# Kernel tuning notes

Measured on AMD Instinct MI355X. Metric: run time of the kernel, lower is better.

Reference implementation:

```python
import jax, jax.numpy as jnp
import numpy as np


def setup_inputs() -> dict:
    key = jax.random.key(0)
    ks = jax.random.split(key, 8)
    B, C, H, W = 4, 512, 64, 64
    O = 64  # output_size for f/g projections
    x = jax.random.normal(ks[0], (B, C, H, W), dtype=jnp.float32)
    s = 0.02
    f_w = jax.random.normal(ks[1], (O, C), dtype=jnp.float32) * s
    f_b = jnp.zeros((O,), dtype=jnp.float32)
    g_w = jax.random.normal(ks[2], (O, C), dtype=jnp.float32) * s
    g_b = jnp.zeros((O,), dtype=jnp.float32)
    h_w = jax.random.normal(ks[3], (C, C), dtype=jnp.float32) * s
    h_b = jnp.zeros((C,), dtype=jnp.float32)
    gamma = jnp.float32(0.5)  # torch init is 0.0; nonzero to exercise the attention path
    return {"x": x, "f_w": f_w, "f_b": f_b, "g_w": g_w, "g_b": g_b,
            "h_w": h_w, "h_b": h_b, "gamma": gamma}


def reference(x, f_w, f_b, g_w, g_b, h_w, h_b, gamma):
    B, C, Hh, Ww = x.shape
    N = Hh * Ww
    # 1x1 convs == per-pixel linear projections
    xf = x.reshape(B, C, N)                                   # [B,C,N]
    f = jnp.einsum('oc,bcn->bon', f_w, xf) + f_b[None, :, None]  # [B,O,N]
    g = jnp.einsum('oc,bcn->bon', g_w, xf) + g_b[None, :, None]  # [B,O,N]
    h = jnp.einsum('oc,bcn->bon', h_w, xf) + h_b[None, :, None]  # [B,C,N]
    # scores[b,i,j] = <f[:, i], g[:, j]>  (f transposed to [B,N,O] then bmm with g)
    scores = jnp.einsum('boi,boj->bij', f, g)                 # [B,N,N]
    # NOTE: original uses nn.Softmax(dim=1) -> normalize over the i (first N) axis
    sm = jax.nn.softmax(scores, axis=1)                       # [B,N,N]
    attn = jnp.einsum('bcn,bnm->bcm', h, sm)                  # [B,C,N]
    out = gamma * attn.reshape(B, C, Hh, Ww) + x
    return out
```

## Files before the change

### kernel.cpp

```cpp
#include <hip/hip_runtime.h>


#define N_PIX 4096
#define C_IN  512

typedef __attribute__((ext_vector_type(8)))  short bf16x8;
typedef __attribute__((ext_vector_type(16))) float f32x16;
typedef __attribute__((ext_vector_type(8)))  int   i32x8;

__device__ __forceinline__ float fexp2(float x) {
    return __builtin_amdgcn_exp2f(x);
}

__device__ inline unsigned int f2bf(float f) {
    union { float f; unsigned u; } x; x.f = f;
    unsigned r = x.u + 0x7FFFu + ((x.u >> 16) & 1u);
    return r >> 16;
}

__device__ __forceinline__ unsigned cvt_pk_bf16(float a, float b) {
#if __has_builtin(__builtin_amdgcn_cvt_pk_bf16_f32)
    auto r = __builtin_amdgcn_cvt_pk_bf16_f32(a, b);
    unsigned u; __builtin_memcpy(&u, &r, 4); return u;
#else
    return f2bf(a) | (f2bf(b) << 16);
#endif
}

__device__ __forceinline__ unsigned pk_fp8x4(float a, float b, float c, float d) {
    int v = 0;
    v = __builtin_amdgcn_cvt_pk_fp8_f32(a, b, v, false);
    v = __builtin_amdgcn_cvt_pk_fp8_f32(c, d, v, true);
    return (unsigned)v;
}

__global__ __launch_bounds__(256) void pack_w(
    const float* __restrict__ f_w, const float* __restrict__ g_w,
    const float* __restrict__ h_w, unsigned short* __restrict__ wall)
{
    __shared__ __align__(16) unsigned short Ls[32 * 520];
    const int t  = threadIdx.x;
    const int tt = blockIdx.x;
    const float* W; int rbase;
    if (tt < 2)      { W = f_w; rbase = tt * 32; }
    else if (tt < 4) { W = g_w; rbase = (tt - 2) * 32; }
    else             { W = h_w; rbase = (tt - 4) * 32; }
    const float fs = (tt < 2) ? 1.442695041f : 1.0f;

    #pragma unroll
    for (int k = 0; k < 16; ++k) {
        const int off = (t + k * 256) * 4;
        const int row = off >> 9, col = off & 511;
        float4 v = *(const float4*)&W[(size_t)(rbase + row) * C_IN + col];
        uint2 pk; pk.x = cvt_pk_bf16(v.x * fs, v.y * fs); pk.y = cvt_pk_bf16(v.z * fs, v.w * fs);
        *(uint2*)&Ls[row * 520 + col] = pk;
    }
    __syncthreads();
    #pragma unroll
    for (int j = 0; j < 8; ++j) {
        const int o = t + j * 256;
        const int q = o >> 6, lq = o & 63;
        const int row = lq & 31, c0 = q * 16 + (lq >> 5) * 8;
        uint4 pk = *(const uint4*)&Ls[row * 520 + c0];
        *(uint4*)&wall[(size_t)tt * 16384 + (size_t)o * 8] = pk;
    }
}

__global__ __launch_bounds__(512, 4) void proj_kernel(
    const float* __restrict__ x,
    const unsigned short* __restrict__ wall,
    const float* __restrict__ f_b, const float* __restrict__ g_b,
    const float* __restrict__ h_b,
    unsigned short* __restrict__ fa, unsigned short* __restrict__ gbuf,
    unsigned char* __restrict__ ha)
{
    __shared__ __align__(16) unsigned short Xf[2][8192];
    const int t    = threadIdx.x;
    const int w    = t >> 6;
    const int l    = t & 63;
    const int half = l >> 5;
    const int tx = t & 15;
    const int ty = t >> 4;
    const int c0 = ty * 2;
    const int qs = c0 >> 4;
    const int woff = (c0 & 7);
    const int hfs = (c0 >> 3) & 1;

    const int blk = blockIdx.x;

    if (blk < 256) {
        const int b  = blk >> 6;
        const int nb = blk & 63;
        const int n0g = nb * 64;
        const int n0 = tx * 4;

        f32x16 acc[2][2];
        #pragma unroll
        for (int j = 0; j < 2; ++j)
            #pragma unroll
            for (int s = 0; s < 2; ++s)
                #pragma unroll
                for (int r = 0; r < 16; ++r) acc[j][s][r] = 0.f;

        const unsigned short* wp0 = wall + (size_t)(4 + w * 2) * 16384 + (size_t)l * 8;
        const unsigned short* wp1 = wp0 + 16384;
        bf16x8 wc0 = *(const bf16x8*)wp0;
        bf16x8 wc1 = *(const bf16x8*)wp1;

        float4 v0 = *(const float4*)&x[((size_t)(b * C_IN + c0)) * N_PIX + n0g + n0];
        float4 v1 = *(const float4*)&x[((size_t)(b * C_IN + c0 + 1)) * N_PIX + n0g + n0];

        for (int it = 0; it < 8; ++it) {
            {
                unsigned short* xb = &Xf[it & 1][0];
                const float a0[4] = {v0.x, v0.y, v0.z, v0.w};
                const float a1[4] = {v1.x, v1.y, v1.z, v1.w};
                #pragma unroll
                for (int j = 0; j < 4; ++j) {
                    const int n = n0 + j;
                    const int off = ((n >> 5) * 4 + qs) * 512
                                  + ((n & 31) + 32 * hfs) * 8 + woff;
                    *(unsigned*)&xb[off] = cvt_pk_bf16(a0[j], a1[j]);
                }
            }
            if (it < 7) {
                v0 = *(const float4*)&x[((size_t)(b * C_IN + (it + 1) * 64 + c0)) * N_PIX + n0g + n0];
                v1 = *(const float4*)&x[((size_t)(b * C_IN + (it + 1) * 64 + c0 + 1)) * N_PIX + n0g + n0];
            }
            __syncthreads();
            const unsigned short* xb = &Xf[it & 1][0];
            #pragma unroll
            for (int q = 0; q < 4; ++q) {
                const int qn = (it * 4 + q + 1) & 31;
                bf16x8 wn0 = *(const bf16x8*)(wp0 + (size_t)qn * 512);
                bf16x8 wn1 = *(const bf16x8*)(wp1 + (size_t)qn * 512);
                bf16x8 x0 = *(const bf16x8*)&xb[(0 * 4 + q) * 512 + l * 8];
                bf16x8 x1 = *(const bf16x8*)&xb[(1 * 4 + q) * 512 + l * 8];
                acc[0][0] = __builtin_amdgcn_mfma_f32_32x32x16_bf16(x0, wc0, acc[0][0], 0, 0, 0);
                acc[0][1] = __builtin_amdgcn_mfma_f32_32x32x16_bf16(x1, wc0, acc[0][1], 0, 0, 0);
                acc[1][0] = __builtin_amdgcn_mfma_f32_32x32x16_bf16(x0, wc1, acc[1][0], 0, 0, 0);
                acc[1][1] = __builtin_amdgcn_mfma_f32_32x32x16_bf16(x1, wc1, acc[1][1], 0, 0, 0);
                wc0 = wn0; wc1 = wn1;
            }
            __syncthreads();
        }

        const int nt_ = nb >> 1, kt_ = nb & 1;
        #pragma unroll
        for (int j = 0; j < 2; ++j) {
            const int ctile = w * 2 + j;
            const int ch = ctile * 32 + (l & 31);
            const float hb = h_b[ch];
            unsigned char* hdst = ha
                + (((size_t)(b * 16 + ctile) * 32 + nt_) * 2 + kt_) * 2048
                + (size_t)(l & 31) * 32 + 16 * half;
            #pragma unroll
            for (int ns = 0; ns < 2; ++ns) {
                uint4 pk4;
                pk4.x = pk_fp8x4(acc[j][ns][0]  + hb, acc[j][ns][1]  + hb,
                                 acc[j][ns][2]  + hb, acc[j][ns][3]  + hb);
                pk4.y = pk_fp8x4(acc[j][ns][4]  + hb, acc[j][ns][5]  + hb,
                                 acc[j][ns][6]  + hb, acc[j][ns][7]  + hb);
                pk4.z = pk_fp8x4(acc[j][ns][8]  + hb, acc[j][ns][9]  + hb,
                                 acc[j][ns][10] + hb, acc[j][ns][11] + hb);
                pk4.w = pk_fp8x4(acc[j][ns][12] + hb, acc[j][ns][13] + hb,
                                 acc[j][ns][14] + hb, acc[j][ns][15] + hb);
                *(uint4*)&hdst[ns * 1024] = pk4;
            }
        }
    } else {
        const int blk2 = blk - 256;
        const int b   = blk2 >> 5;
        const int nb2 = blk2 & 31;
        const int n0g = nb2 * 128;
        const int tt    = w & 3;
        const int npair = w >> 2;

        f32x16 acc[2];
        #pragma unroll
        for (int s = 0; s < 2; ++s)
            #pragma unroll
            for (int r = 0; r < 16; ++r) acc[s][r] = 0.f;

        const unsigned short* wpf = wall + (size_t)tt * 16384 + (size_t)l * 8;
        bf16x8 wcf = *(const bf16x8*)wpf;

        float4 v00 = *(const float4*)&x[((size_t)(b * C_IN + c0)) * N_PIX + n0g + tx * 4];
        float4 v10 = *(const float4*)&x[((size_t)(b * C_IN + c0 + 1)) * N_PIX + n0g + tx * 4];
        float4 v01 = *(const float4*)&x[((size_t)(b * C_IN + c0)) * N_PIX + n0g + 64 + tx * 4];
        float4 v11 = *(const float4*)&x[((size_t)(b * C_IN + c0 + 1)) * N_PIX + n0g + 64 + tx * 4];

        for (int it = 0; it < 8; ++it) {
            {
                unsigned short* xb = &Xf[it & 1][0];
                const float a00[4] = {v00.x, v00.y, v00.z, v00.w};
                const float a10[4] = {v10.x, v10.y, v10.z, v10.w};
                const float a01[4] = {v01.x, v01.y, v01.z, v01.w};
                const float a11[4] = {v11.x, v11.y, v11.z, v11.w};
                #pragma unroll
                for (int j = 0; j < 4; ++j) {
                    const int n = tx * 4 + j;
                    const int off0 = ((n >> 5) * 4 + qs) * 512
                                   + ((n & 31) + 32 * hfs) * 8 + woff;
                    *(unsigned*)&xb[off0] = cvt_pk_bf16(a00[j], a10[j]);
                    const int n2 = 64 + n;
                    const int off1 = ((n2 >> 5) * 4 + qs) * 512
                                   + ((n2 & 31) + 32 * hfs) * 8 + woff;
                    *(unsigned*)&xb[off1] = cvt_pk_bf16(a01[j], a11[j]);
                }
            }
            if (it < 7) {
                const size_t rb = (size_t)(b * C_IN + (it + 1) * 64 + c0) * N_PIX + n0g;
                v00 = *(const float4*)&x[rb + tx * 4];
                v10 = *(const float4*)&x[rb + N_PIX + tx * 4];
                v01 = *(const float4*)&x[rb + 64 + tx * 4];
                v11 = *(const float4*)&x[rb + N_PIX + 64 + tx * 4];
            }
            __syncthreads();
            const unsigned short* xb = &Xf[it & 1][0];
            #pragma unroll
            for (int q = 0; q < 4; ++q) {
                const int qn = (it * 4 + q + 1) & 31;
                bf16x8 wnf = *(const bf16x8*)(wpf + (size_t)qn * 512);
                bf16x8 x0 = *(const bf16x8*)&xb[((npair * 2 + 0) * 4 + q) * 512 + l * 8];
                bf16x8 x1 = *(const bf16x8*)&xb[((npair * 2 + 1) * 4 + q) * 512 + l * 8];
                acc[0] = __builtin_amdgcn_mfma_f32_32x32x16_bf16(wcf, x0, acc[0], 0, 0, 0);
                acc[1] = __builtin_amdgcn_mfma_f32_32x32x16_bf16(wcf, x1, acc[1], 0, 0, 0);
                wcf = wnf;
            }
            __syncthreads();
        }

        unsigned short* buf = (tt < 2) ? fa : gbuf;
        const float* bias = (tt < 2) ? f_b : g_b;
        const float bscale = (tt < 2) ? 1.442695041f : 1.0f;
        #pragma unroll
        for (int s = 0; s < 2; ++s) {
            const int ntile = nb2 * 4 + npair * 2 + s;
            #pragma unroll
            for (int j2 = 0; j2 < 4; ++j2) {
                const int o_base = (tt & 1) * 32 + 8 * j2 + 4 * half;
                float4 bv = *(const float4*)&bias[o_base];
                bv.x *= bscale; bv.y *= bscale; bv.z *= bscale; bv.w *= bscale;
                const int q  = o_base >> 4;
                const int lp = (l & 31) + 32 * (j2 & 1);
                uint2 pk;
                pk.x = cvt_pk_bf16(acc[s][4 * j2 + 0] + bv.x, acc[s][4 * j2 + 1] + bv.y);
                pk.y = cvt_pk_bf16(acc[s][4 * j2 + 2] + bv.z, acc[s][4 * j2 + 3] + bv.w);
                size_t off = (((size_t)(b * 128 + ntile) * 4 + q) * 64 + lp) * 8 + 4 * half;
                *(uint2*)&buf[off] = pk;
            }
        }
    }
}

__global__ __launch_bounds__(512, 4) void attn_kernel(
    const unsigned short* __restrict__ fa,
    const unsigned short* __restrict__ gbuf,
    const unsigned char* __restrict__ ha,
    const float* __restrict__ x,
    const float* __restrict__ gamma_p,
    float* __restrict__ out)
{
    __shared__ __align__(16) unsigned char Ebuf[2][64 * 136];
    __shared__ float den_part[4][64];
    __shared__ float den_inv[64];

    const int t    = threadIdx.x;
    const int w    = t >> 6;
    const int l    = t & 63;
    const int lane = l & 31;
    const int half = l >> 5;
    const int nsub = w & 3;
    const int mt   = w >> 2;

    const int blk   = blockIdx.x;
    const int chalf = blk & 1;
    const int b     = (blk >> 1) & 3;
    const int mi    = blk >> 3;
    const int m0    = mi * 64;

    bf16x8 gfrag[4];
    {
        const unsigned short* gp = gbuf
            + ((size_t)(b * 128 + mi * 2 + mt) * 4) * 512 + (size_t)l * 8;
        #pragma unroll
        for (int q = 0; q < 4; ++q)
            gfrag[q] = *(const bf16x8*)(gp + (size_t)q * 512);
    }

    f32x16 acc[2];
    #pragma unroll
    for (int j = 0; j < 2; ++j)
        #pragma unroll
        for (int r = 0; r < 16; ++r) acc[j][r] = 0.f;

    float denp = 0.f;

    const unsigned short* fptr = fa + (size_t)b * (128 * 4) * 512
                               + (size_t)(nsub * 4) * 512 + (size_t)l * 8;
    const int ctg = chalf * 8 + w;
    const unsigned char* hptr = ha
        + (size_t)(b * 16 + ctg) * 131072 + (size_t)l * 32;

    bf16x8 ff[4];
    #pragma unroll
    for (int q = 0; q < 4; ++q)
        ff[q] = *(const bf16x8*)(fptr + (size_t)q * 512);
    fptr += 8192;
    i32x8 h0 = *(const i32x8*)hptr;
    i32x8 h1 = *(const i32x8*)(hptr + 2048);
    hptr += 4096;

    {
        f32x16 s;
        #pragma unroll
        for (int r = 0; r < 16; ++r) s[r] = 0.f;
        #pragma unroll
        for (int q = 0; q < 4; ++q)
            s = __builtin_amdgcn_mfma_f32_32x32x16_bf16(ff[q], gfrag[q], s, 0, 0, 0);
        #pragma unroll
        for (int q = 0; q < 4; ++q)
            ff[q] = *(const bf16x8*)(fptr + (size_t)q * 512);
        fptr += 8192;
        unsigned pkv[4];
        #pragma unroll
        for (int r4 = 0; r4 < 4; ++r4) {
            float e0 = fexp2(fminf(s[r4 * 4 + 0] - 8.656170f, 8.656170f));
            float e1 = fexp2(fminf(s[r4 * 4 + 1] - 8.656170f, 8.656170f));
            float e2 = fexp2(fminf(s[r4 * 4 + 2] - 8.656170f, 8.656170f));
            float e3 = fexp2(fminf(s[r4 * 4 + 3] - 8.656170f, 8.656170f));
            denp += (e0 + e1) + (e2 + e3);
            pkv[r4] = pk_fp8x4(e0, e1, e2, e3);
        }
        unsigned char* ew = &Ebuf[0][(mt * 32 + lane) * 136 + nsub * 32 + half * 16];
        *(unsigned long long*)(ew)     = (unsigned long long)pkv[0]
                                       | ((unsigned long long)pkv[1] << 32);
        *(unsigned long long*)(ew + 8) = (unsigned long long)pkv[2]
                                       | ((unsigned long long)pkv[3] << 32);
    }
    __builtin_amdgcn_sched_barrier(0);
    asm volatile("s_waitcnt lgkmcnt(0)" ::: "memory");
    __builtin_amdgcn_s_barrier();
    __builtin_amdgcn_sched_barrier(0);

    for (int nt = 0; nt < 31; ++nt) {
        __builtin_amdgcn_s_setprio(1);
        f32x16 s;
        #pragma unroll
        for (int r = 0; r < 16; ++r) s[r] = 0.f;
        #pragma unroll
        for (int q = 0; q < 4; ++q)
            s = __builtin_amdgcn_mfma_f32_32x32x16_bf16(ff[q], gfrag[q], s, 0, 0, 0);
        #pragma unroll
        for (int q = 0; q < 4; ++q)
            ff[q] = *(const bf16x8*)(fptr + (size_t)q * 512);
        fptr += 8192;

        const unsigned char* eb = &Ebuf[nt & 1][0];
        #pragma unroll
        for (int kt = 0; kt < 2; ++kt) {
            const unsigned char* e0p = eb + lane * 136 + kt * 64 + half * 32;
            union { i32x8 v; long d[4]; } b0, b1;
            #pragma unroll
            for (int j = 0; j < 4; ++j) {
                b0.d[j] = *(const long*)(e0p + 8 * j);
                b1.d[j] = *(const long*)(e0p + 32 * 136 + 8 * j);
            }
            const i32x8 av = kt ? h1 : h0;
            acc[0] = __builtin_amdgcn_mfma_scale_f32_32x32x64_f8f6f4(
                av, b0.v, acc[0], 0, 0, 0, 127, 0, 127);
            acc[1] = __builtin_amdgcn_mfma_scale_f32_32x32x64_f8f6f4(
                av, b1.v, acc[1], 0, 0, 0, 127, 0, 127);
        }
        __builtin_amdgcn_s_setprio(0);
        h0 = *(const i32x8*)hptr;
        h1 = *(const i32x8*)(hptr + 2048);
        hptr += 4096;

        unsigned pkv[4];
        #pragma unroll
        for (int r4 = 0; r4 < 4; ++r4) {
            float e0 = fexp2(fminf(s[r4 * 4 + 0] - 8.656170f, 8.656170f));
            float e1 = fexp2(fminf(s[r4 * 4 + 1] - 8.656170f, 8.656170f));
            float e2 = fexp2(fminf(s[r4 * 4 + 2] - 8.656170f, 8.656170f));
            float e3 = fexp2(fminf(s[r4 * 4 + 3] - 8.656170f, 8.656170f));
            denp += (e0 + e1) + (e2 + e3);
            pkv[r4] = pk_fp8x4(e0, e1, e2, e3);
        }
        {
            unsigned char* ew = &Ebuf[(nt + 1) & 1][(mt * 32 + lane) * 136 + nsub * 32 + half * 16];
            *(unsigned long long*)(ew)     = (unsigned long long)pkv[0]
                                           | ((unsigned long long)pkv[1] << 32);
            *(unsigned long long*)(ew + 8) = (unsigned long long)pkv[2]
                                           | ((unsigned long long)pkv[3] << 32);
        }

        __builtin_amdgcn_sched_barrier(0);
        asm volatile("s_waitcnt lgkmcnt(0)" ::: "memory");
        __builtin_amdgcn_s_barrier();
        __builtin_amdgcn_sched_barrier(0);
    }

    {
        const unsigned char* eb = &Ebuf[31 & 1][0];
        #pragma unroll
        for (int kt = 0; kt < 2; ++kt) {
            const unsigned char* e0p = eb + lane * 136 + kt * 64 + half * 32;
            union { i32x8 v; long d[4]; } b0, b1;
            #pragma unroll
            for (int j = 0; j < 4; ++j) {
                b0.d[j] = *(const long*)(e0p + 8 * j);
                b1.d[j] = *(const long*)(e0p + 32 * 136 + 8 * j);
            }
            const i32x8 av = kt ? h1 : h0;
            acc[0] = __builtin_amdgcn_mfma_scale_f32_32x32x64_f8f6f4(
                av, b0.v, acc[0], 0, 0, 0, 127, 0, 127);
            acc[1] = __builtin_amdgcn_mfma_scale_f32_32x32x64_f8f6f4(
                av, b1.v, acc[1], 0, 0, 0, 127, 0, 127);
        }
    }

    denp += __shfl_xor(denp, 32, 64);
    if (l < 32) den_part[nsub][mt * 32 + lane] = denp;
    __syncthreads();
    if (t < 64) {
        float d = den_part[0][t] + den_part[1][t] + den_part[2][t] + den_part[3][t];
        den_inv[t] = 1.0f / d;
    }
    __syncthreads();

    const float gs = gamma_p[0];
    #pragma unroll
    for (int mt2 = 0; mt2 < 2; ++mt2) {
        const int mloc = mt2 * 32 + lane;
        const float dinv = den_inv[mloc];
        const int m = m0 + mloc;
        #pragma unroll
        for (int r = 0; r < 16; ++r) {
            const int c = ctg * 32 + (r & 3) + ((r >> 2) * 8) + half * 4;
            const size_t idx = ((size_t)(b * C_IN + c)) * N_PIX + m;
            out[idx] = gs * acc[mt2][r] * dinv + x[idx];
        }
    }
}

extern "C" void kernel_launch(void* const* d_in, const int* in_sizes, int n_in,
                              void* d_out, int out_size, void* d_ws, size_t ws_size,
                              hipStream_t stream)
{
    const float* x     = (const float*)d_in[0];
    const float* f_w   = (const float*)d_in[1];
    const float* f_b   = (const float*)d_in[2];
    const float* g_w   = (const float*)d_in[3];
    const float* g_b   = (const float*)d_in[4];
    const float* h_w   = (const float*)d_in[5];
    const float* h_b   = (const float*)d_in[6];
    const float* gamma = (const float*)d_in[7];
    float* out = (float*)d_out;

    unsigned short* fa   = (unsigned short*)d_ws;
    unsigned short* gbuf = fa + (1u << 20);
    unsigned char*  ha   = (unsigned char*)(gbuf + (1u << 20));
    unsigned short* wall = (unsigned short*)(ha + (8u << 20));

    pack_w<<<20, 256, 0, stream>>>(f_w, g_w, h_w, wall);

    proj_kernel<<<384, 512, 0, stream>>>(x, wall, f_b, g_b, h_b, fa, gbuf, ha);

    attn_kernel<<<512, 512, 0, stream>>>(fa, gbuf, ha, x, gamma, out);
}
```

Baseline: 169.7 us.

## Drop second barrier in proj loop, shrink LDS, split fg projection blocks, remove exp clamp

The projection kernel's double-buffered X tile loop now uses one raw barrier per iteration instead of two __syncthreads. The LDS buffer is halved to 64 pixels per block, and the f/g projection path now covers 64 pixels per block with one MFMA accumulator instead of 128, so the grid grows from 384 to 512 blocks. The attention kernel drops the fminf clamp before exp2, saving ALU work but allowing overflow or saturation in the fp8 exp values if scores exceed the assumed maximum. Removing the second barrier relies on the double buffer to avoid a write-after-read race between iterations.

```diff
diff --git a/kernel.cpp b/kernel.cpp
--- a/kernel.cpp
+++ b/kernel.cpp
@@ -33,6 +33,13 @@
     v = __builtin_amdgcn_cvt_pk_fp8_f32(c, d, v, true);
     return (unsigned)v;
 }
+
+#define RAW_BARRIER() do { \
+    __builtin_amdgcn_sched_barrier(0); \
+    asm volatile("s_waitcnt lgkmcnt(0)" ::: "memory"); \
+    __builtin_amdgcn_s_barrier(); \
+    __builtin_amdgcn_sched_barrier(0); \
+} while (0)
 
 __global__ __launch_bounds__(256) void pack_w(
     const float* __restrict__ f_w, const float* __restrict__ g_w,
@@ -74,7 +81,7 @@
     unsigned short* __restrict__ fa, unsigned short* __restrict__ gbuf,
     unsigned char* __restrict__ ha)
 {
-    __shared__ __align__(16) unsigned short Xf[2][8192];
+    __shared__ __align__(16) unsigned short Xf[2][4096];
     const int t    = threadIdx.x;
     const int w    = t >> 6;
     const int l    = t & 63;
@@ -127,7 +134,7 @@
                 v0 = *(const float4*)&x[((size_t)(b * C_IN + (it + 1) * 64 + c0)) * N_PIX + n0g + n0];
                 v1 = *(const float4*)&x[((size_t)(b * C_IN + (it + 1) * 64 + c0 + 1)) * N_PIX + n0g + n0];
             }
-            __syncthreads();
+            RAW_BARRIER();
             const unsigned short* xb = &Xf[it & 1][0];
             #pragma unroll
             for (int q = 0; q < 4; ++q) {
@@ -142,7 +149,6 @@
                 acc[1][1] = __builtin_amdgcn_mfma_f32_32x32x16_bf16(x1, wc1, acc[1][1], 0, 0, 0);
                 wc0 = wn0; wc1 = wn1;
             }
-            __syncthreads();
         }
 
         const int nt_ = nb >> 1, kt_ = nb & 1;
@@ -170,86 +176,68 @@
         }
     } else {
         const int blk2 = blk - 256;
-        const int b   = blk2 >> 5;
-        const int nb2 = blk2 & 31;
-        const int n0g = nb2 * 128;
+        const int b   = blk2 >> 6;
+        const int nb2 = blk2 & 63;
+        const int n0g = nb2 * 64;
+        const int n0 = tx * 4;
         const int tt    = w & 3;
         const int npair = w >> 2;
 
-        f32x16 acc[2];
-        #pragma unroll
-        for (int s = 0; s < 2; ++s)
-            #pragma unroll
-            for (int r = 0; r < 16; ++r) acc[s][r] = 0.f;
+        f32x16 acc;
+        #pragma unroll
+        for (int r = 0; r < 16; ++r) acc[r] = 0.f;
 
         const unsigned short* wpf = wall + (size_t)tt * 16384 + (size_t)l * 8;
         bf16x8 wcf = *(const bf16x8*)wpf;
 
-        float4 v00 = *(const float4*)&x[((size_t)(b * C_IN + c0)) * N_PIX + n0g + tx * 4];
-        float4 v10 = *(const float4*)&x[((size_t)(b * C_IN + c0 + 1)) * N_PIX + n0g + tx * 4];
-        float4 v01 = *(const float4*)&x[((size_t)(b * C_IN + c0)) * N_PIX + n0g + 64 + tx * 4];
-        float4 v11 = *(const float4*)&x[((size_t)(b * C_IN + c0 + 1)) * N_PIX + n0g + 64 + tx * 4];
+        float4 v0 = *(const float4*)&x[((size_t)(b * C_IN + c0)) * N_PIX + n0g + n0];
+        float4 v1 = *(const float4*)&x[((size_t)(b * C_IN + c0 + 1)) * N_PIX + n0g + n0];
 
         for (int it = 0; it < 8; ++it) {
             {
                 unsigned short* xb = &Xf[it & 1][0];
-                const float a00[4] = {v00.x, v00.y, v00.z, v00.w};
-                const float a10[4] = {v10.x, v10.y, v10.z, v10.w};
-                const float a01[4] = {v01.x, v01.y, v01.z, v01.w};
-                const float a11[4] = {v11.x, v11.y, v11.z, v11.w};
+                const float a0[4] = {v0.x, v0.y, v0.z, v0.w};
+                const float a1[4] = {v1.x, v1.y, v1.z, v1.w};
                 #pragma unroll
                 for (int j = 0; j < 4; ++j) {
-                    const int n = tx * 4 + j;
-                    const int off0 = ((n >> 5) * 4 + qs) * 512
-                                   + ((n & 31) + 32 * hfs) * 8 + woff;
-                    *(unsigned*)&xb[off0] = cvt_pk_bf16(a00[j], a10[j]);
-                    const int n2 = 64 + n;
-                    const int off1 = ((n2 >> 5) * 4 + qs) * 512
-                                   + ((n2 & 31) + 32 * hfs) * 8 + woff;
-                    *(unsigned*)&xb[off1] = cvt_pk_bf16(a01[j], a11[j]);
+                    const int n = n0 + j;
+                    const int off = ((n >> 5) * 4 + qs) * 512
+                                  + ((n & 31) + 32 * hfs) * 8 + woff;
+                    *(unsigned*)&xb[off] = cvt_pk_bf16(a0[j], a1[j]);
                 }
             }
             if (it < 7) {
-                const size_t rb = (size_t)(b * C_IN + (it + 1) * 64 + c0) * N_PIX + n0g;
-                v00 = *(const float4*)&x[rb + tx * 4];
-                v10 = *(const float4*)&x[rb + N_PIX + tx * 4];
-                v01 = *(const float4*)&x[rb + 64 + tx * 4];
-                v11 = *(const float4*)&x[rb + N_PIX + 64 + tx * 4];
-            }
-            __syncthreads();
+                v0 = *(const float4*)&x[((size_t)(b * C_IN + (it + 1) * 64 + c0)) * N_PIX + n0g + n0];
+                v1 = *(const float4*)&x[((size_t)(b * C_IN + (it + 1) * 64 + c0 + 1)) * N_PIX + n0g + n0];
+            }
+            RAW_BARRIER();
             const unsigned short* xb = &Xf[it & 1][0];
             #pragma unroll
             for (int q = 0; q < 4; ++q) {
                 const int qn = (it * 4 + q + 1) & 31;
                 bf16x8 wnf = *(const bf16x8*)(wpf + (size_t)qn * 512);
-                bf16x8 x0 = *(const bf16x8*)&xb[((npair * 2 + 0) * 4 + q) * 512 + l * 8];
-                bf16x8 x1 = *(const bf16x8*)&xb[((npair * 2 + 1) * 4 + q) * 512 + l * 8];
-                acc[0] = __builtin_amdgcn_mfma_f32_32x32x16_bf16(wcf, x0, acc[0], 0, 0, 0);
-                acc[1] = __builtin_amdgcn_mfma_f32_32x32x16_bf16(wcf, x1, acc[1], 0, 0, 0);
+                bf16x8 x0 = *(const bf16x8*)&xb[(npair * 4 + q) * 512 + l * 8];
+                acc = __builtin_amdgcn_mfma_f32_32x32x16_bf16(wcf, x0, acc, 0, 0, 0);
                 wcf = wnf;
             }
-            __syncthreads();
         }
 
         unsigned short* buf = (tt < 2) ? fa : gbuf;
         const float* bias = (tt < 2) ? f_b : g_b;
         const float bscale = (tt < 2) ? 1.442695041f : 1.0f;
-        #pragma unroll
-        for (int s = 0; s < 2; ++s) {
-            const int ntile = nb2 * 4 + npair * 2 + s;
-            #pragma unroll
-            for (int j2 = 0; j2 < 4; ++j2) {
-                const int o_base = (tt & 1) * 32 + 8 * j2 + 4 * half;
-                float4 bv = *(const float4*)&bias[o_base];
-                bv.x *= bscale; bv.y *= bscale; bv.z *= bscale; bv.w *= bscale;
-                const int q  = o_base >> 4;
-                const int lp = (l & 31) + 32 * (j2 & 1);
-                uint2 pk;
-                pk.x = cvt_pk_bf16(acc[s][4 * j2 + 0] + bv.x, acc[s][4 * j2 + 1] + bv.y);
-                pk.y = cvt_pk_bf16(acc[s][4 * j2 + 2] + bv.z, acc[s][4 * j2 + 3] + bv.w);
-                size_t off = (((size_t)(b * 128 + ntile) * 4 + q) * 64 + lp) * 8 + 4 * half;
-                *(uint2*)&buf[off] = pk;
-            }
+        const int ntile = nb2 * 2 + npair;
+        #pragma unroll
+        for (int j2 = 0; j2 < 4; ++j2) {
+            const int o_base = (tt & 1) * 32 + 8 * j2 + 4 * half;
+            float4 bv = *(const float4*)&bias[o_base];
+            bv.x *= bscale; bv.y *= bscale; bv.z *= bscale; bv.w *= bscale;
+            const int q  = o_base >> 4;
+            const int lp = (l & 31) + 32 * (j2 & 1);
+            uint2 pk;
+            pk.x = cvt_pk_bf16(acc[4 * j2 + 0] + bv.x, acc[4 * j2 + 1] + bv.y);
+            pk.y = cvt_pk_bf16(acc[4 * j2 + 2] + bv.z, acc[4 * j2 + 3] + bv.w);
+            size_t off = (((size_t)(b * 128 + ntile) * 4 + q) * 64 + lp) * 8 + 4 * half;
+            *(uint2*)&buf[off] = pk;
         }
     }
 }
@@ -326,10 +314,10 @@
         unsigned pkv[4];
         #pragma unroll
         for (int r4 = 0; r4 < 4; ++r4) {
-            float e0 = fexp2(fminf(s[r4 * 4 + 0] - 8.656170f, 8.656170f));
-            float e1 = fexp2(fminf(s[r4 * 4 + 1] - 8.656170f, 8.656170f));
-            float e2 = fexp2(fminf(s[r4 * 4 + 2] - 8.656170f, 8.656170f));
-            float e3 = fexp2(fminf(s[r4 * 4 + 3] - 8.656170f, 8.656170f));
+            float e0 = fexp2(s[r4 * 4 + 0] - 8.656170f);
+            float e1 = fexp2(s[r4 * 4 + 1] - 8.656170f);
+            float e2 = fexp2(s[r4 * 4 + 2] - 8.656170f);
+            float e3 = fexp2(s[r4 * 4 + 3] - 8.656170f);
             denp += (e0 + e1) + (e2 + e3);
             pkv[r4] = pk_fp8x4(e0, e1, e2, e3);
         }
@@ -339,10 +327,7 @@
         *(unsigned long long*)(ew + 8) = (unsigned long long)pkv[2]
                                        | ((unsigned long long)pkv[3] << 32);
     }
-    __builtin_amdgcn_sched_barrier(0);
-    asm volatile("s_waitcnt lgkmcnt(0)" ::: "memory");
-    __builtin_amdgcn_s_barrier();
-    __builtin_amdgcn_sched_barrier(0);
+    RAW_BARRIER();
 
     for (int nt = 0; nt < 31; ++nt) {
         __builtin_amdgcn_s_setprio(1);
@@ -381,10 +366,10 @@
         unsigned pkv[4];
         #pragma unroll
         for (int r4 = 0; r4 < 4; ++r4) {
-            float e0 = fexp2(fminf(s[r4 * 4 + 0] - 8.656170f, 8.656170f));
-            float e1 = fexp2(fminf(s[r4 * 4 + 1] - 8.656170f, 8.656170f));
-            float e2 = fexp2(fminf(s[r4 * 4 + 2] - 8.656170f, 8.656170f));
-            float e3 = fexp2(fminf(s[r4 * 4 + 3] - 8.656170f, 8.656170f));
+            float e0 = fexp2(s[r4 * 4 + 0] - 8.656170f);
+            float e1 = fexp2(s[r4 * 4 + 1] - 8.656170f);
+            float e2 = fexp2(s[r4 * 4 + 2] - 8.656170f);
+            float e3 = fexp2(s[r4 * 4 + 3] - 8.656170f);
             denp += (e0 + e1) + (e2 + e3);
             pkv[r4] = pk_fp8x4(e0, e1, e2, e3);
         }
@@ -396,10 +381,7 @@
                                            | ((unsigned long long)pkv[3] << 32);
         }
 
-        __builtin_amdgcn_sched_barrier(0);
-        asm volatile("s_waitcnt lgkmcnt(0)" ::: "memory");
-        __builtin_amdgcn_s_barrier();
-        __builtin_amdgcn_sched_barrier(0);
+        RAW_BARRIER();
     }
 
     {
@@ -466,7 +448,7 @@
 
     pack_w<<<20, 256, 0, stream>>>(f_w, g_w, h_w, wall);
 
-    proj_kernel<<<384, 512, 0, stream>>>(x, wall, f_b, g_b, h_b, fa, gbuf, ha);
+    proj_kernel<<<512, 512, 0, stream>>>(x, wall, f_b, g_b, h_b, fa, gbuf, ha);
 
     attn_kernel<<<512, 512, 0, stream>>>(fa, gbuf, ha, x, gamma, out);
 }
```

After: 169.2 us. About the same (-0.3%).
